# Kernel optimization log

Hardware: AMD Instinct MI355X
Metric: run time of the kernel (lower is better)

Reference implementation:

```python
import jax, jax.numpy as jnp
import numpy as np


def setup_inputs() -> dict:
    key = jax.random.key(0)
    k1, k2, k3, k4, k5 = jax.random.split(key, 5)
    num_seqs, num_heads, head_dim = 64, 32, 128
    num_blocks, num_kv_heads, block_size = 4096, 8, 16
    max_blocks = 128  # max context = 128 * 16 = 2048 tokens
    query = jax.random.normal(k1, (num_seqs, num_heads, head_dim), dtype=jnp.float32)
    key_cache = jax.random.normal(k2, (num_blocks, num_kv_heads, block_size, head_dim), dtype=jnp.float32)
    value_cache = jax.random.normal(k3, (num_blocks, num_kv_heads, block_size, head_dim), dtype=jnp.float32)
    block_tables = jax.random.randint(k4, (num_seqs, max_blocks), 0, num_blocks, dtype=jnp.int32)
    context_lens = jax.random.randint(k5, (num_seqs,), 1, max_blocks * block_size + 1, dtype=jnp.int32)
    return {
        "query": query,
        "key_cache": key_cache,
        "value_cache": value_cache,
        "block_tables": block_tables,
        "context_lens": context_lens,
    }


def reference(query, key_cache, value_cache, block_tables, context_lens):
    # Paged-attention decode (torch fallback path of zAttention.decode).
    S, H, D = query.shape
    NB, KVH, BS, _ = key_cache.shape
    G = H // KVH            # GQA factor: query heads per KV head
    MB = block_tables.shape[1]
    L = MB * BS             # padded max context length
    scale = 1.0 / jnp.sqrt(jnp.asarray(D, dtype=query.dtype))

    # Gather paged KV blocks per sequence: [S, MB, KVH, BS, D]
    k = key_cache[block_tables]
    v = value_cache[block_tables]
    # -> [S, KVH, L, D]
    k = k.transpose(0, 2, 1, 3, 4).reshape(S, KVH, L, D)
    v = v.transpose(0, 2, 1, 3, 4).reshape(S, KVH, L, D)

    # Group query heads by KV head: [S, KVH, G, D]
    q = query.reshape(S, KVH, G, D)

    # scores: [S, KVH, G, L]
    scores = jnp.einsum("sgqd,sgkd->sgqk", q, k) * scale
    valid = jnp.arange(L)[None, None, None, :] < context_lens[:, None, None, None]
    scores = jnp.where(valid, scores, -jnp.inf)
    probs = jax.nn.softmax(scores, axis=-1)

    out = jnp.einsum("sgqk,sgkd->sgqd", probs, v)  # [S, KVH, G, D]
    return out.reshape(S, H, D)
```

## Files before the change

kernel.cpp:

```cpp
#include <hip/hip_runtime.h>
#include <hip/hip_bf16.h>
#include <math.h>

#define S_   64
#define H_   32
#define D_   128
#define KVH_ 8
#define G_   4
#define BS_  16
#define MB_  128
#define LMAX_ 2048
#define TB_  4

#define SCALE_ 0.08838834764831845f

__global__ __launch_bounds__(256, 4)
void pa_partial(const float* __restrict__ q,
                const float* __restrict__ kc,
                const float* __restrict__ vc,
                const int* __restrict__ bt,
                const int* __restrict__ cl,
                float* __restrict__ ws,
                int PART, int maxP)
{
    const int s    = blockIdx.z;
    const int kvh  = blockIdx.y;
    const int part = blockIdx.x;

    const int len = cl[s];
    const int t0  = part * PART;
    if (t0 >= len) return;
    const int t1 = min(t0 + PART, len);

    const int tid  = threadIdx.x;
    const int gid  = tid >> 5;
    const int lane = tid & 31;

    const int nblk = PART >> 7;

    float4 qv[G_];
#pragma unroll
    for (int g = 0; g < G_; ++g)
        qv[g] = *(const float4*)(q + ((size_t)(s * H_ + kvh * G_ + g)) * D_ + lane * 4);

    float  m[G_], l[G_];
    float4 acc[G_];
#pragma unroll
    for (int g = 0; g < G_; ++g) {
        m[g] = -INFINITY; l[g] = 0.f;
        acc[g] = make_float4(0.f, 0.f, 0.f, 0.f);
    }

    const int* btr = bt + s * MB_;
    const size_t kvh_off = (size_t)kvh * (BS_ * D_);

    for (int b = 0; b < nblk; ++b) {
        const int tblk = t0 + (gid * nblk + b) * BS_;
        if (tblk >= t1) break;
        const int bid = btr[tblk >> 4];
        const float* kb = kc + (size_t)bid * (KVH_ * BS_ * D_) + kvh_off + lane * 4;
        const float* vb = vc + (size_t)bid * (KVH_ * BS_ * D_) + kvh_off + lane * 4;
        const int tend = min(tblk + BS_, t1);

#pragma unroll
        for (int tbi = 0; tbi < BS_ / TB_; ++tbi) {
            const int tb = tblk + tbi * TB_;
            if (tb >= tend) break;

            float4 k4[TB_], v4[TB_];
#pragma unroll
            for (int i = 0; i < TB_; ++i) {
                k4[i] = *(const float4*)(kb + (size_t)(tbi * TB_ + i) * D_);
                v4[i] = *(const float4*)(vb + (size_t)(tbi * TB_ + i) * D_);
            }

            float sc[TB_][G_];
#pragma unroll
            for (int i = 0; i < TB_; ++i)
#pragma unroll
                for (int g = 0; g < G_; ++g)
                    sc[i][g] = qv[g].x * k4[i].x + qv[g].y * k4[i].y +
                               qv[g].z * k4[i].z + qv[g].w * k4[i].w;

#pragma unroll
            for (int off = 16; off; off >>= 1)
#pragma unroll
                for (int i = 0; i < TB_; ++i)
#pragma unroll
                    for (int g = 0; g < G_; ++g)
                        sc[i][g] += __shfl_xor(sc[i][g], off, 32);

#pragma unroll
            for (int i = 0; i < TB_; ++i) {
                const bool valid = (tb + i) < t1;
#pragma unroll
                for (int g = 0; g < G_; ++g)
                    sc[i][g] = valid ? sc[i][g] * SCALE_ : -INFINITY;
            }

#pragma unroll
            for (int g = 0; g < G_; ++g) {
                const float smax = fmaxf(fmaxf(sc[0][g], sc[1][g]),
                                         fmaxf(sc[2][g], sc[3][g]));
                const float mn   = fmaxf(m[g], smax);
                const float corr = __expf(m[g] - mn);
                const float p0 = __expf(sc[0][g] - mn);
                const float p1 = __expf(sc[1][g] - mn);
                const float p2 = __expf(sc[2][g] - mn);
                const float p3 = __expf(sc[3][g] - mn);
                l[g] = l[g] * corr + ((p0 + p1) + (p2 + p3));
                acc[g].x = acc[g].x * corr + p0 * v4[0].x + p1 * v4[1].x + p2 * v4[2].x + p3 * v4[3].x;
                acc[g].y = acc[g].y * corr + p0 * v4[0].y + p1 * v4[1].y + p2 * v4[2].y + p3 * v4[3].y;
                acc[g].z = acc[g].z * corr + p0 * v4[0].z + p1 * v4[1].z + p2 * v4[2].z + p3 * v4[3].z;
                acc[g].w = acc[g].w * corr + p0 * v4[0].w + p1 * v4[1].w + p2 * v4[2].w + p3 * v4[3].w;
                m[g] = mn;
            }
        }
    }

    __shared__ float lm[8][G_];
    __shared__ float ll[8][G_];
    __shared__ float lacc[8][G_][D_];

#pragma unroll
    for (int g = 0; g < G_; ++g) {
        if (lane == 0) { lm[gid][g] = m[g]; ll[gid][g] = l[g]; }
        *(float4*)&lacc[gid][g][lane * 4] = acc[g];
    }
    __syncthreads();

    float* pbase = ws + (((size_t)(s * KVH_ + kvh) * maxP + part) * G_) * 130;
#pragma unroll
    for (int i = 0; i < 2; ++i) {
        const int idx = tid + 256 * i;
        const int g = idx >> 7;
        const int d = idx & 127;
        float M = lm[0][g];
#pragma unroll
        for (int r = 1; r < 8; ++r) M = fmaxf(M, lm[r][g]);
        float L = 0.f, val = 0.f;
#pragma unroll
        for (int r = 0; r < 8; ++r) {
            const float w = __expf(lm[r][g] - M);
            L   += w * ll[r][g];
            val += w * lacc[r][g][d];
        }
        float* pb = pbase + (size_t)g * 130;
        if (d == 0) { pb[0] = M; pb[1] = L; }
        pb[2 + d] = val;
    }
}

__global__ __launch_bounds__(128)
void pa_combine(const float* __restrict__ ws,
                const int* __restrict__ cl,
                float* __restrict__ out,
                int PART, int maxP)
{
    const int h = blockIdx.x;
    const int s = blockIdx.y;
    const int kvh = h >> 2;
    const int g   = h & 3;
    const int d   = threadIdx.x;

    const int len = cl[s];
    const int np  = (len + PART - 1) / PART;

    const float* base = ws + ((size_t)(s * KVH_ + kvh) * maxP) * (G_ * 130) + (size_t)g * 130;

    float M = -INFINITY;
    for (int p = 0; p < np; ++p) M = fmaxf(M, base[(size_t)p * (G_ * 130)]);

    float L = 0.f, val = 0.f;
    for (int p = 0; p < np; ++p) {
        const float* pb = base + (size_t)p * (G_ * 130);
        const float w = __expf(pb[0] - M);
        L   += w * pb[1];
        val += w * pb[2 + d];
    }
    out[((size_t)s * H_ + h) * D_ + d] = val / L;
}

extern "C" void kernel_launch(void* const* d_in, const int* in_sizes, int n_in,
                              void* d_out, int out_size, void* d_ws, size_t ws_size,
                              hipStream_t stream)
{
    const float* q  = (const float*)d_in[0];
    const float* kc = (const float*)d_in[1];
    const float* vc = (const float*)d_in[2];
    const int*   bt = (const int*)d_in[3];
    const int*   cl = (const int*)d_in[4];
    float* out = (float*)d_out;
    float* ws  = (float*)d_ws;

    int PART = 128;
    int maxP = LMAX_ / PART;
    while (PART < LMAX_) {
        size_t need = (size_t)S_ * KVH_ * maxP * G_ * 130 * sizeof(float);
        if (need <= ws_size) break;
        PART *= 2; maxP = LMAX_ / PART;
    }

    dim3 grid1(maxP, KVH_, S_);
    pa_partial<<<grid1, 256, 0, stream>>>(q, kc, vc, bt, cl, ws, PART, maxP);

    dim3 grid2(H_, S_);
    pa_combine<<<grid2, 128, 0, stream>>>(ws, cl, out, PART, maxP);
}
```

Before: 142.8 us.

## Double-buffer KV loads per warp over two pages and enlarge partitions

Each warp now handles a fixed 32-token span (two pages) and prefetches the next 4-token group of K and V into registers while computing the current one. The partition size doubles, so there are fewer partial blocks and less combine work, and the occupancy hint is removed from launch bounds. The goal is to hide global memory latency behind computation. In exchange it uses more registers, and the per-warp span is hardcoded, so it silently assumes the partition size stays at 256.

```diff
diff --git a/kernel.cpp b/kernel.cpp
--- a/kernel.cpp
+++ b/kernel.cpp
@@ -10,11 +10,10 @@
 #define BS_  16
 #define MB_  128
 #define LMAX_ 2048
-#define TB_  4
 
 #define SCALE_ 0.08838834764831845f
 
-__global__ __launch_bounds__(256, 4)
+__global__ __launch_bounds__(256)
 void pa_partial(const float* __restrict__ q,
                 const float* __restrict__ kc,
                 const float* __restrict__ vc,
@@ -36,8 +35,6 @@
     const int gid  = tid >> 5;
     const int lane = tid & 31;
 
-    const int nblk = PART >> 7;
-
     float4 qv[G_];
 #pragma unroll
     for (int g = 0; g < G_; ++g)
@@ -54,48 +51,64 @@
     const int* btr = bt + s * MB_;
     const size_t kvh_off = (size_t)kvh * (BS_ * D_);
 
-    for (int b = 0; b < nblk; ++b) {
-        const int tblk = t0 + (gid * nblk + b) * BS_;
-        if (tblk >= t1) break;
-        const int bid = btr[tblk >> 4];
-        const float* kb = kc + (size_t)bid * (KVH_ * BS_ * D_) + kvh_off + lane * 4;
-        const float* vb = vc + (size_t)bid * (KVH_ * BS_ * D_) + kvh_off + lane * 4;
-        const int tend = min(tblk + BS_, t1);
-
-#pragma unroll
-        for (int tbi = 0; tbi < BS_ / TB_; ++tbi) {
-            const int tb = tblk + tbi * TB_;
-            if (tb >= tend) break;
-
-            float4 k4[TB_], v4[TB_];
-#pragma unroll
-            for (int i = 0; i < TB_; ++i) {
-                k4[i] = *(const float4*)(kb + (size_t)(tbi * TB_ + i) * D_);
-                v4[i] = *(const float4*)(vb + (size_t)(tbi * TB_ + i) * D_);
+    const int t_base  = t0 + gid * 32;
+    const int navail  = t1 - t_base;
+
+    if (navail > 0) {
+        const int page0 = t_base >> 4;
+        const int bid0  = btr[page0];
+        const int bid1  = btr[page0 + 1];
+        const float* kp0 = kc + (size_t)bid0 * (KVH_ * BS_ * D_) + kvh_off + lane * 4;
+        const float* vp0 = vc + (size_t)bid0 * (KVH_ * BS_ * D_) + kvh_off + lane * 4;
+        const float* kp1 = kc + (size_t)bid1 * (KVH_ * BS_ * D_) + kvh_off + lane * 4;
+        const float* vp1 = vc + (size_t)bid1 * (KVH_ * BS_ * D_) + kvh_off + lane * 4;
+
+        const int nb = min(8, (navail + 3) >> 2);
+
+        float4 kb[2][4], vb[2][4];
+#pragma unroll
+        for (int r = 0; r < 4; ++r) {
+            kb[0][r] = *(const float4*)(kp0 + (size_t)r * D_);
+            vb[0][r] = *(const float4*)(vp0 + (size_t)r * D_);
+        }
+
+#pragma unroll
+        for (int i = 0; i < 8; ++i) {
+            if (i >= nb) break;
+            const int cur = i & 1, nxt = cur ^ 1;
+
+            if (i + 1 < nb) {
+                const float* kpp = ((i + 1) < 4 ? kp0 : kp1) + (size_t)(((i + 1) & 3) * 4) * D_;
+                const float* vpp = ((i + 1) < 4 ? vp0 : vp1) + (size_t)(((i + 1) & 3) * 4) * D_;
+#pragma unroll
+                for (int r = 0; r < 4; ++r) {
+                    kb[nxt][r] = *(const float4*)(kpp + (size_t)r * D_);
+                    vb[nxt][r] = *(const float4*)(vpp + (size_t)r * D_);
+                }
             }
 
-            float sc[TB_][G_];
-#pragma unroll
-            for (int i = 0; i < TB_; ++i)
+            float sc[4][G_];
+#pragma unroll
+            for (int i2 = 0; i2 < 4; ++i2)
 #pragma unroll
                 for (int g = 0; g < G_; ++g)
-                    sc[i][g] = qv[g].x * k4[i].x + qv[g].y * k4[i].y +
-                               qv[g].z * k4[i].z + qv[g].w * k4[i].w;
+                    sc[i2][g] = qv[g].x * kb[cur][i2].x + qv[g].y * kb[cur][i2].y +
+                                qv[g].z * kb[cur][i2].z + qv[g].w * kb[cur][i2].w;
 
 #pragma unroll
             for (int off = 16; off; off >>= 1)
 #pragma unroll
-                for (int i = 0; i < TB_; ++i)
+                for (int i2 = 0; i2 < 4; ++i2)
 #pragma unroll
                     for (int g = 0; g < G_; ++g)
-                        sc[i][g] += __shfl_xor(sc[i][g], off, 32);
-
-#pragma unroll
-            for (int i = 0; i < TB_; ++i) {
-                const bool valid = (tb + i) < t1;
+                        sc[i2][g] += __shfl_xor(sc[i2][g], off, 32);
+
+#pragma unroll
+            for (int i2 = 0; i2 < 4; ++i2) {
+                const bool valid = (i * 4 + i2) < navail;
 #pragma unroll
                 for (int g = 0; g < G_; ++g)
-                    sc[i][g] = valid ? sc[i][g] * SCALE_ : -INFINITY;
+                    sc[i2][g] = valid ? sc[i2][g] * SCALE_ : -INFINITY;
             }
 
 #pragma unroll
@@ -109,10 +122,10 @@
                 const float p2 = __expf(sc[2][g] - mn);
                 const float p3 = __expf(sc[3][g] - mn);
                 l[g] = l[g] * corr + ((p0 + p1) + (p2 + p3));
-                acc[g].x = acc[g].x * corr + p0 * v4[0].x + p1 * v4[1].x + p2 * v4[2].x + p3 * v4[3].x;
-                acc[g].y = acc[g].y * corr + p0 * v4[0].y + p1 * v4[1].y + p2 * v4[2].y + p3 * v4[3].y;
-                acc[g].z = acc[g].z * corr + p0 * v4[0].z + p1 * v4[1].z + p2 * v4[2].z + p3 * v4[3].z;
-                acc[g].w = acc[g].w * corr + p0 * v4[0].w + p1 * v4[1].w + p2 * v4[2].w + p3 * v4[3].w;
+                acc[g].x = acc[g].x * corr + p0 * vb[cur][0].x + p1 * vb[cur][1].x + p2 * vb[cur][2].x + p3 * vb[cur][3].x;
+                acc[g].y = acc[g].y * corr + p0 * vb[cur][0].y + p1 * vb[cur][1].y + p2 * vb[cur][2].y + p3 * vb[cur][3].y;
+                acc[g].z = acc[g].z * corr + p0 * vb[cur][0].z + p1 * vb[cur][1].z + p2 * vb[cur][2].z + p3 * vb[cur][3].z;
+                acc[g].w = acc[g].w * corr + p0 * vb[cur][0].w + p1 * vb[cur][1].w + p2 * vb[cur][2].w + p3 * vb[cur][3].w;
                 m[g] = mn;
             }
         }
@@ -193,7 +206,7 @@
     float* out = (float*)d_out;
     float* ws  = (float*)d_ws;
 
-    int PART = 128;
+    int PART = 256;
     int maxP = LMAX_ / PART;
     while (PART < LMAX_) {
         size_t need = (size_t)S_ * KVH_ * maxP * G_ * 130 * sizeof(float);
```

Result: no change. 140.8 us (-1.4%).
